# Kernel tuning notes

Measured on AMD Instinct MI355X. Metric: run time of the kernel, lower is better.

## Reference

```python
import jax, jax.numpy as jnp
import numpy as np


def setup_inputs() -> dict:
    key = jax.random.key(0)
    k1, k2 = jax.random.split(key)
    B, C, H, W = 32, 256, 64, 64
    data = jax.random.normal(k1, (B, C, H, W), dtype=jnp.float32)
    offset = jax.random.normal(k2, (B, 2, H, W), dtype=jnp.float32)
    trans_std = jnp.float32(0.005)  # learned scalar Parameter
    return {"data": data, "offset": offset, "trans_std": trans_std}


def reference(data, offset, trans_std):
    """Offset-driven bilinear interpolation sampling + global average pooling.

    data:   [B, C, H, W]
    offset: [B, 2, H, W]  (dy, dx) displacement field, scaled by trans_std
    Returns pooled features [B, C].
    """
    B, C, H, W = data.shape
    ts = jnp.clip(trans_std, 0.001, 0.01)  # forward clamps trans_std to [0.001, 0.01]

    # sampling coordinates: base grid + scaled offsets (offsets normalized by H/W)
    ii = jnp.arange(H, dtype=data.dtype)[:, None]   # [H,1]
    jj = jnp.arange(W, dtype=data.dtype)[None, :]   # [1,W]
    y = jnp.clip(ii + ts * offset[:, 0] * H, 0.0, H - 1)  # [B,H,W]
    x = jnp.clip(jj + ts * offset[:, 1] * W, 0.0, W - 1)  # [B,H,W]

    y0 = jnp.clip(jnp.floor(y).astype(jnp.int32), 0, H - 2)
    x0 = jnp.clip(jnp.floor(x).astype(jnp.int32), 0, W - 2)
    y1 = y0 + 1
    x1 = x0 + 1
    wy = y - y0.astype(data.dtype)  # [B,H,W] in [0,1]
    wx = x - x0.astype(data.dtype)

    def sample_one(d, yy0, yy1, xx0, xx1):
        # d: [C,H,W]; index maps: [H,W] -> gathered [C,H,W]
        v00 = d[:, yy0, xx0]
        v01 = d[:, yy0, xx1]
        v10 = d[:, yy1, xx0]
        v11 = d[:, yy1, xx1]
        return v00, v01, v10, v11

    v00, v01, v10, v11 = jax.vmap(sample_one)(data, y0, y1, x0, x1)  # each [B,C,H,W]

    wy_ = wy[:, None]  # broadcast over channels -> [B,1,H,W]
    wx_ = wx[:, None]
    sampled = ((1 - wy_) * (1 - wx_) * v00 + (1 - wy_) * wx_ * v01
               + wy_ * (1 - wx_) * v10 + wy_ * wx_ * v11)  # [B,C,H,W]

    # pooling: global average over spatial locations -> [B,C]
    return jnp.mean(sampled, axis=(2, 3))
```

## Files before the change

### kernel.cpp

```cpp
#include <hip/hip_runtime.h>

#define BATCH 32
#define CHAN  256
#define HGT   64
#define WID   64
#define HW    4096

__global__ __launch_bounds__(1024) void weight_map_kernel(
        const float* __restrict__ offset,
        const float* __restrict__ ts_ptr,
        float* __restrict__ A)
{
    const int b   = blockIdx.x;
    const int tid = threadIdx.x;

    __shared__ float acc[HW];
    acc[tid]        = 0.0f;
    acc[tid + 1024] = 0.0f;
    acc[tid + 2048] = 0.0f;
    acc[tid + 3072] = 0.0f;
    __syncthreads();

    float ts = ts_ptr[0];
    ts = fminf(fmaxf(ts, 0.001f), 0.01f);

    const float* off_y = offset + (size_t)b * 2 * HW;
    const float* off_x = off_y + HW;

    #pragma unroll
    for (int it = 0; it < 4; ++it) {
        const int p = tid + it * 1024;
        const int i = p >> 6;
        const int j = p & 63;
        const float dy = off_y[p];
        const float dx = off_x[p];
        float y = fminf(fmaxf((float)i + ts * dy * 64.0f, 0.0f), 63.0f);
        float x = fminf(fmaxf((float)j + ts * dx * 64.0f, 0.0f), 63.0f);
        int y0 = (int)floorf(y); y0 = min(max(y0, 0), HGT - 2);
        int x0 = (int)floorf(x); x0 = min(max(x0, 0), WID - 2);
        const float wy = y - (float)y0;
        const float wx = x - (float)x0;
        const int base = (y0 << 6) + x0;
        atomicAdd(&acc[base],           (1.0f - wy) * (1.0f - wx));
        atomicAdd(&acc[base + 1],       (1.0f - wy) * wx);
        atomicAdd(&acc[base + WID],     wy * (1.0f - wx));
        atomicAdd(&acc[base + WID + 1], wy * wx);
    }
    __syncthreads();

    float* Ab = A + (size_t)b * HW;
    const float s = 1.0f / (float)HW;
    Ab[tid]        = acc[tid]        * s;
    Ab[tid + 1024] = acc[tid + 1024] * s;
    Ab[tid + 2048] = acc[tid + 2048] * s;
    Ab[tid + 3072] = acc[tid + 3072] * s;
}

__global__ __launch_bounds__(256) void dot_kernel(
        const float* __restrict__ data,
        const float* __restrict__ A,
        float* __restrict__ out)
{
    const int blk   = blockIdx.x;
    const int b     = blk >> 7;
    const int cpair = (blk & 127) << 1;
    const int tid   = threadIdx.x;

    const float* plane0 = data + ((size_t)b * CHAN + cpair) * HW;
    const float* plane1 = plane0 + HW;
    const float* Ab     = A + (size_t)b * HW;

    float s0 = 0.0f, s1 = 0.0f;
    #pragma unroll
    for (int it = 0; it < 4; ++it) {
        const int idx = (it * 256 + tid) * 4;
        const float4 av = *reinterpret_cast<const float4*>(Ab + idx);
        const float4 d0 = *reinterpret_cast<const float4*>(plane0 + idx);
        const float4 d1 = *reinterpret_cast<const float4*>(plane1 + idx);
        s0 = fmaf(av.x, d0.x, s0); s0 = fmaf(av.y, d0.y, s0);
        s0 = fmaf(av.z, d0.z, s0); s0 = fmaf(av.w, d0.w, s0);
        s1 = fmaf(av.x, d1.x, s1); s1 = fmaf(av.y, d1.y, s1);
        s1 = fmaf(av.z, d1.z, s1); s1 = fmaf(av.w, d1.w, s1);
    }

    #pragma unroll
    for (int off = 32; off > 0; off >>= 1) {
        s0 += __shfl_down(s0, off, 64);
        s1 += __shfl_down(s1, off, 64);
    }

    __shared__ float wsum[4][2];
    const int lane = tid & 63;
    const int wv   = tid >> 6;
    if (lane == 0) { wsum[wv][0] = s0; wsum[wv][1] = s1; }
    __syncthreads();
    if (tid < 2) {
        out[(b << 8) + cpair + tid] =
            wsum[0][tid] + wsum[1][tid] + wsum[2][tid] + wsum[3][tid];
    }
}

extern "C" void kernel_launch(void* const* d_in, const int* in_sizes, int n_in,
                              void* d_out, int out_size, void* d_ws, size_t ws_size,
                              hipStream_t stream) {
    const float* data   = (const float*)d_in[0];
    const float* offset = (const float*)d_in[1];
    const float* ts     = (const float*)d_in[2];

    float* A   = (float*)d_ws;
    float* out = (float*)d_out;

    weight_map_kernel<<<BATCH, 1024, 0, stream>>>(offset, ts, A);
    dot_kernel<<<(BATCH * CHAN) / 2, 256, 0, stream>>>(data, A, out);
}
```

Before: 210.6 us.

## Stage weight map in LDS and assign one channel per wavefront

```diff
diff --git a/kernel.cpp b/kernel.cpp
--- a/kernel.cpp
+++ b/kernel.cpp
@@ -56,48 +56,62 @@
     Ab[tid + 3072] = acc[tid + 3072] * s;
 }
 
-__global__ __launch_bounds__(256) void dot_kernel(
+__global__ __launch_bounds__(256, 4) void dot_kernel(
         const float* __restrict__ data,
         const float* __restrict__ A,
         float* __restrict__ out)
 {
-    const int blk   = blockIdx.x;
-    const int b     = blk >> 7;
-    const int cpair = (blk & 127) << 1;
-    const int tid   = threadIdx.x;
+    const int blk = blockIdx.x;
+    const int b   = blk >> 6;
+    const int tid = threadIdx.x;
+    const int w   = tid >> 6;
+    const int lane = tid & 63;
 
-    const float* plane0 = data + ((size_t)b * CHAN + cpair) * HW;
-    const float* plane1 = plane0 + HW;
-    const float* Ab     = A + (size_t)b * HW;
+    __shared__ __align__(16) float As[HW];
 
-    float s0 = 0.0f, s1 = 0.0f;
+    {
+        const float* Ab = A + (size_t)b * HW;
+        #pragma unroll
+        for (int s = 0; s < 4; ++s) {
+            const int idx = (s * 256 + tid) * 4;
+            *reinterpret_cast<float4*>(As + idx) =
+                *reinterpret_cast<const float4*>(Ab + idx);
+        }
+    }
+    __syncthreads();
+
+    const float* plane = data + (size_t)(blk * 4 + w) * HW;
+
+    float4 d[16];
     #pragma unroll
-    for (int it = 0; it < 4; ++it) {
-        const int idx = (it * 256 + tid) * 4;
-        const float4 av = *reinterpret_cast<const float4*>(Ab + idx);
-        const float4 d0 = *reinterpret_cast<const float4*>(plane0 + idx);
-        const float4 d1 = *reinterpret_cast<const float4*>(plane1 + idx);
-        s0 = fmaf(av.x, d0.x, s0); s0 = fmaf(av.y, d0.y, s0);
-        s0 = fmaf(av.z, d0.z, s0); s0 = fmaf(av.w, d0.w, s0);
-        s1 = fmaf(av.x, d1.x, s1); s1 = fmaf(av.y, d1.y, s1);
-        s1 = fmaf(av.z, d1.z, s1); s1 = fmaf(av.w, d1.w, s1);
+    for (int s = 0; s < 16; ++s)
+        d[s] = *reinterpret_cast<const float4*>(plane + s * 256 + lane * 4);
+
+    float a0 = 0.0f, a1 = 0.0f, a2 = 0.0f, a3 = 0.0f;
+    #pragma unroll
+    for (int s = 0; s < 16; ++s) {
+        const float4 av = *reinterpret_cast<const float4*>(As + s * 256 + lane * 4);
+        if ((s & 3) == 0) {
+            a0 = fmaf(av.x, d[s].x, a0); a0 = fmaf(av.y, d[s].y, a0);
+            a0 = fmaf(av.z, d[s].z, a0); a0 = fmaf(av.w, d[s].w, a0);
+        } else if ((s & 3) == 1) {
+            a1 = fmaf(av.x, d[s].x, a1); a1 = fmaf(av.y, d[s].y, a1);
+            a1 = fmaf(av.z, d[s].z, a1); a1 = fmaf(av.w, d[s].w, a1);
+        } else if ((s & 3) == 2) {
+            a2 = fmaf(av.x, d[s].x, a2); a2 = fmaf(av.y, d[s].y, a2);
+            a2 = fmaf(av.z, d[s].z, a2); a2 = fmaf(av.w, d[s].w, a2);
+        } else {
+            a3 = fmaf(av.x, d[s].x, a3); a3 = fmaf(av.y, d[s].y, a3);
+            a3 = fmaf(av.z, d[s].z, a3); a3 = fmaf(av.w, d[s].w, a3);
+        }
     }
+    float sum = (a0 + a1) + (a2 + a3);
 
     #pragma unroll
-    for (int off = 32; off > 0; off >>= 1) {
-        s0 += __shfl_down(s0, off, 64);
-        s1 += __shfl_down(s1, off, 64);
-    }
+    for (int off = 32; off > 0; off >>= 1)
+        sum += __shfl_down(sum, off, 64);
 
-    __shared__ float wsum[4][2];
-    const int lane = tid & 63;
-    const int wv   = tid >> 6;
-    if (lane == 0) { wsum[wv][0] = s0; wsum[wv][1] = s1; }
-    __syncthreads();
-    if (tid < 2) {
-        out[(b << 8) + cpair + tid] =
-            wsum[0][tid] + wsum[1][tid] + wsum[2][tid] + wsum[3][tid];
-    }
+    if (lane == 0) out[blk * 4 + w] = sum;
 }
 
 extern "C" void kernel_launch(void* const* d_in, const int* in_sizes, int n_in,
@@ -111,5 +125,5 @@
     float* out = (float*)d_out;
 
     weight_map_kernel<<<BATCH, 1024, 0, stream>>>(offset, ts, A);
-    dot_kernel<<<(BATCH * CHAN) / 2, 256, 0, stream>>>(data, A, out);
+    dot_kernel<<<(BATCH * CHAN) / 4, 256, 0, stream>>>(data, A, out);
 }
```

Result: no change. 212.5 us (+0.9%).
